# Kernel tuning notes

Hardware: AMD Instinct MI355X
Metric: run time of the kernel (lower is better)

Reference implementation:

```python
import jax, jax.numpy as jnp
import numpy as np
import math

D = 768      # d_model
H = 12       # heads
DH = D // H  # per-head dim
HID = 3072   # ffn hidden
L = 6        # layers each for encoder/decoder
S = 1024     # encoder seq len
T = 1024     # decoder seq len
MAXLEN = 1024


def pos_encoding(d, length):
    # pe[pos, 2i] = sin(pos / scale**i), pe[pos, 2i+1] = cos(pos / scale**i), scale = 1000**(2/d)
    scale = 1000.0 ** (2.0 / d)
    inv = scale ** (-np.arange(d // 2, dtype=np.float64))
    ang = np.arange(length, dtype=np.float64)[:, None] * inv[None, :]
    pe = np.zeros((length, d), dtype=np.float32)
    pe[:, 0::2] = np.sin(ang)
    pe[:, 1::2] = np.cos(ang)
    return jnp.asarray(pe)


def setup_inputs() -> dict:
    key = jax.random.key(0)
    ks = iter(jax.random.split(key, 64))
    def nrm(shape, s=0.02):
        return jax.random.normal(next(ks), shape, dtype=jnp.float32) * s
    inp = {
        'xl': nrm((S, D), 1.0),
        'dl': nrm((T, D), 1.0),
        'pos_enc': pos_encoding(D, MAXLEN),
        # encoder params (stacked over L layers, heads stacked over H)
        'enc_wq': nrm((L, H, DH, D)), 'enc_wk': nrm((L, H, DH, D)), 'enc_wv': nrm((L, H, DH, D)),
        'enc_wo': nrm((L, D, D)), 'enc_bo': jnp.zeros((L, D), jnp.float32),
        'enc_ln_a': jnp.ones((L, 2, D), jnp.float32), 'enc_ln_b': jnp.zeros((L, 2, D), jnp.float32),
        'enc_w1': nrm((L, HID, D)), 'enc_b1': jnp.zeros((L, HID), jnp.float32),
        'enc_w2': nrm((L, D, HID)), 'enc_b2': jnp.zeros((L, D), jnp.float32),
        # decoder self-attention
        'dec_wq': nrm((L, H, DH, D)), 'dec_wk': nrm((L, H, DH, D)), 'dec_wv': nrm((L, H, DH, D)),
        'dec_wo': nrm((L, D, D)), 'dec_bo': jnp.zeros((L, D), jnp.float32),
        # decoder cross-attention
        'dec_cwq': nrm((L, H, DH, D)), 'dec_cwk': nrm((L, H, DH, D)), 'dec_cwv': nrm((L, H, DH, D)),
        'dec_cwo': nrm((L, D, D)), 'dec_cbo': jnp.zeros((L, D), jnp.float32),
        'dec_ln_a': jnp.ones((L, 3, D), jnp.float32), 'dec_ln_b': jnp.zeros((L, 3, D), jnp.float32),
        'dec_w1': nrm((L, HID, D)), 'dec_b1': jnp.zeros((L, HID), jnp.float32),
        'dec_w2': nrm((L, D, HID)), 'dec_b2': jnp.zeros((L, D), jnp.float32),
    }
    return inp


def _ln_res(x, fx, a, b, eps=1e-6):
    # x = x + fx; a*(x-mean)/(std+eps)+b with UNBIASED std (torch default) and std (not var) in denom
    x = x + fx
    m = x.mean(-1, keepdims=True)
    s = jnp.std(x, axis=-1, keepdims=True, ddof=1)
    return a * (x - m) / (s + eps) + b


def _mha(qx, kx, vx, wq, wk, wv, wo, bo, mask=None):
    q = jnp.einsum('sd,hed->hse', qx, wq)  # [H,S,dh]
    k = jnp.einsum('td,hed->hte', kx, wk)
    v = jnp.einsum('td,hed->hte', vx, wv)
    scores = jnp.einsum('hse,hte->hst', q, k) / math.sqrt(q.shape[-1])
    if mask is not None:
        scores = scores + mask
    p = jax.nn.softmax(scores, axis=-1)  # softmax over keys (torch dim=1 on 2D scores)
    o = jnp.einsum('hst,hte->hse', p, v)
    o = jnp.transpose(o, (1, 0, 2)).reshape(qx.shape[0], -1)  # concat heads
    return o @ wo.T + bo


def _ffn(x, w1, b1, w2, b2):
    return jax.nn.relu(x @ w1.T + b1) @ w2.T + b2


def reference(xl, dl, pos_enc, enc_wq, enc_wk, enc_wv, enc_wo, enc_bo, enc_ln_a, enc_ln_b,
              enc_w1, enc_b1, enc_w2, enc_b2,
              dec_wq, dec_wk, dec_wv, dec_wo, dec_bo,
              dec_cwq, dec_cwk, dec_cwv, dec_cwo, dec_cbo,
              dec_ln_a, dec_ln_b, dec_w1, dec_b1, dec_w2, dec_b2):
    m = xl + pos_enc[: xl.shape[0]]
    for l in range(L):
        fx = _mha(m, m, m, enc_wq[l], enc_wk[l], enc_wv[l], enc_wo[l], enc_bo[l])
        m = _ln_res(m, fx, enc_ln_a[l, 0], enc_ln_b[l, 0])
        fx = _ffn(m, enc_w1[l], enc_b1[l], enc_w2[l], enc_b2[l])
        m = _ln_res(m, fx, enc_ln_a[l, 1], enc_ln_b[l, 1])
    n = dl.shape[0]
    # additive causal mask: -10000 where j > i
    cmask = -10000.0 * (jnp.arange(n)[None, :] > jnp.arange(n)[:, None]).astype(jnp.float32)
    out = dl + pos_enc[:n]
    for l in range(L):
        fx = _mha(out, out, out, dec_wq[l], dec_wk[l], dec_wv[l], dec_wo[l], dec_bo[l], cmask)
        out = _ln_res(out, fx, dec_ln_a[l, 0], dec_ln_b[l, 0])
        fx = _mha(out, m, m, dec_cwq[l], dec_cwk[l], dec_cwv[l], dec_cwo[l], dec_cbo[l])
        out = _ln_res(out, fx, dec_ln_a[l, 1], dec_ln_b[l, 1])
        fx = _ffn(out, dec_w1[l], dec_b1[l], dec_w2[l], dec_b2[l])
        out = _ln_res(out, fx, dec_ln_a[l, 2], dec_ln_b[l, 2])
    return jax.nn.softmax(out, axis=1)
```

## Files before the change

### kernel.cpp

```cpp
#include <hip/hip_runtime.h>
#include <math.h>

#define DMODEL 768
#define NHEAD 12
#define DHEAD 64
#define HIDDEN 3072
#define NLAYER 6
#define SEQ 1024
#define AC_ELEMS (SEQ * DMODEL)

typedef unsigned short u16;
typedef __attribute__((ext_vector_type(8))) short short8;
typedef __attribute__((ext_vector_type(4))) float f32x4;

__device__ __forceinline__ u16 f2bf(float f) {
    union { float f; unsigned u; } v; v.f = f;
    unsigned u = v.u;
    return (u16)((u + 0x7fffu + ((u >> 16) & 1u)) >> 16);
}
__device__ __forceinline__ float bf2f(u16 b) {
    union { unsigned u; float f; } v; v.u = ((unsigned)b) << 16; return v.f;
}

__device__ __forceinline__ void async16(const void* g, void* l) {
    __builtin_amdgcn_global_load_lds(
        (const __attribute__((address_space(1))) unsigned int*)g,
        (__attribute__((address_space(3))) unsigned int*)l, 16, 0, 0);
}

template<int N> __device__ __forceinline__ void waitv() {
    asm volatile("s_waitcnt vmcnt(%0)" :: "n"(N) : "memory");
    __builtin_amdgcn_sched_barrier(0);
}
__device__ __forceinline__ void drain_all() {
    asm volatile("s_waitcnt vmcnt(0) lgkmcnt(0)" ::: "memory");
    __builtin_amdgcn_sched_barrier(0);
}
__device__ __forceinline__ void bar() {
    __builtin_amdgcn_sched_barrier(0);
    __builtin_amdgcn_s_barrier();
    __builtin_amdgcn_sched_barrier(0);
}

__device__ __forceinline__ float block_sum(float v, float* red) {
    int tid = threadIdx.x;
    red[tid] = v;
    __syncthreads();
#pragma unroll
    for (int s = 128; s > 0; s >>= 1) {
        if (tid < s) red[tid] += red[tid + s];
        __syncthreads();
    }
    float r = red[0];
    __syncthreads();
    return r;
}
__device__ __forceinline__ float block_max(float v, float* red) {
    int tid = threadIdx.x;
    red[tid] = v;
    __syncthreads();
#pragma unroll
    for (int s = 128; s > 0; s >>= 1) {
        if (tid < s) red[tid] = fmaxf(red[tid], red[tid + s]);
        __syncthreads();
    }
    float r = red[0];
    __syncthreads();
    return r;
}

__global__ __launch_bounds__(256) void add_pe(const float* __restrict__ a,
                                              const float* __restrict__ b,
                                              float* __restrict__ o,
                                              u16* __restrict__ ob, int n) {
    int i = blockIdx.x * 256 + threadIdx.x;
    if (i < n) { float v = a[i] + b[i]; o[i] = v; ob[i] = f2bf(v); }
}

__global__ __launch_bounds__(256) void cvt_bf16(const float* __restrict__ src,
                                                u16* __restrict__ dst,
                                                long long per, long long sls, long long dls) {
    long long i = ((long long)blockIdx.x * 256 + threadIdx.x) * 4;
    if (i >= per) return;
    const float* s = src + (long long)blockIdx.y * sls + i;
    u16* d = dst + (long long)blockIdx.y * dls + i;
    float4 v = *(const float4*)s;
    ushort4 o;
    o.x = f2bf(v.x); o.y = f2bf(v.y); o.z = f2bf(v.z); o.w = f2bf(v.w);
    *(ushort4*)d = o;
}

template<int TM, int TN, int WR, int WC>
__global__ __launch_bounds__(WR * WC * 64) void gemm_mfma(
    const u16* __restrict__ A, int lda,
    const void* __restrict__ Bp, int ldb, int b_f32,
    const float* __restrict__ bias,
    void* __restrict__ Cp, int ldc, int c_bf16,
    float* __restrict__ C2,
    u16* __restrict__ vt_out, int vt_col0,
    int Ksub, int relu)
{
    constexpr int T  = WR * WC * 64;
    constexpr bool MW = (WR * WC) > 1;
    constexpr int FM = TM / (WR * 16), FN = TN / (WC * 16);
    constexpr int NA = TM * 8 / T, NB = TN * 8 / T;
    constexpr int LPS = NA + NB;
    __shared__ __align__(16) u16 As[3][TM * 64];
    __shared__ __align__(16) u16 Bs[3][TN * 64];

    const int zs = blockIdx.z;
    const u16*   B16 = (const u16*)Bp   + (long long)zs * Ksub;
    const float* B32 = (const float*)Bp + (long long)zs * Ksub;
    A += (long long)zs * Ksub;
    u16*   C16 = (u16*)Cp;
    float* C32 = (float*)Cp;

    const int t = threadIdx.x, lane = t & 63, w = t >> 6;
    const int wy = w / WC, wx = w % WC;
    const int n0 = blockIdx.y * TM, m0 = blockIdx.x * TN;

    auto stage = [&](int b, int k0) {
#pragma unroll
        for (int i = 0; i < NA; ++i) {
            int L = i * T + t;
            int row = L >> 3, cp = L & 7, c = cp ^ (row & 7);
            async16(A + (long long)(n0 + row) * lda + k0 + (c << 3),
                    &As[b][(i * T + w * 64) * 8]);
        }
        if (!b_f32) {
#pragma unroll
            for (int i = 0; i < NB; ++i) {
                int L = i * T + t;
                int row = L >> 3, cp = L & 7, c = cp ^ (row & 7);
                async16(B16 + (long long)(m0 + row) * ldb + k0 + (c << 3),
                        &Bs[b][(i * T + w * 64) * 8]);
            }
        } else {
#pragma unroll
            for (int i = 0; i < NB; ++i) {
                int L = i * T + t;
                int row = L >> 3, cp = L & 7, c = cp ^ (row & 7);
                const float* s = B32 + (long long)(m0 + row) * ldb + k0 + (c << 3);
                float4 x = *(const float4*)s;
                float4 y = *(const float4*)(s + 4);
                uint4 pk;
                pk.x = (unsigned)f2bf(x.x) | ((unsigned)f2bf(x.y) << 16);
                pk.y = (unsigned)f2bf(x.z) | ((unsigned)f2bf(x.w) << 16);
                pk.z = (unsigned)f2bf(y.x) | ((unsigned)f2bf(y.y) << 16);
                pk.w = (unsigned)f2bf(y.z) | ((unsigned)f2bf(y.w) << 16);
                *(uint4*)&Bs[b][row * 64 + cp * 8] = pk;
            }
        }
    };

    const int nk = Ksub / 64;
    stage(0, 0);
    if (nk > 1) stage(1, 64);

    f32x4 acc[FM][FN] = {};

    for (int tt = 0; tt < nk; ++tt) {
        if (tt + 2 < nk) stage((tt + 2) % 3, (tt + 2) * 64);
        if (b_f32)             drain_all();
        else if (tt + 2 < nk)  waitv<2 * LPS>();
        else if (tt + 1 < nk)  waitv<LPS>();
        else                   waitv<0>();
        if (MW) bar();

        const u16* Ac = As[tt % 3];
        const u16* Bc = Bs[tt % 3];
#pragma unroll
        for (int kk = 0; kk < 2; ++kk) {
            short8 af[FM], bfv[FN];
            const int cb = kk * 4 + (lane >> 4);
#pragma unroll
            for (int m = 0; m < FM; ++m) {
                int R = wy * (TM / WR) + m * 16 + (lane & 15);
                af[m] = *(const short8*)&Ac[R * 64 + ((cb ^ (R & 7)) << 3)];
            }
#pragma unroll
            for (int n = 0; n < FN; ++n) {
                int R = wx * (TN / WC) + n * 16 + (lane & 15);
                bfv[n] = *(const short8*)&Bc[R * 64 + ((cb ^ (R & 7)) << 3)];
            }
#pragma unroll
            for (int m = 0; m < FM; ++m)
#pragma unroll
                for (int n = 0; n < FN; ++n)
                    acc[m][n] = __builtin_amdgcn_mfma_f32_16x16x32_bf16(af[m], bfv[n], acc[m][n], 0, 0, 0);
        }
        if (MW) bar();
    }

    const int cj = lane & 15, ci0 = (lane >> 4) << 2;
    const bool z0 = (zs == 0);
#pragma unroll
    for (int m = 0; m < FM; ++m) {
#pragma unroll
        for (int n = 0; n < FN; ++n) {
            int col = m0 + wx * (TN / WC) + n * 16 + cj;
            bool to_vt = z0 && vt_out && (col >= vt_col0);
            float bv = (z0 && bias) ? bias[col] : 0.0f;
#pragma unroll
            for (int r = 0; r < 4; ++r) {
                int row = n0 + wy * (TM / WR) + m * 16 + ci0 + r;
                float v = acc[m][n][r] + bv;
                if (relu) v = fmaxf(v, 0.0f);
                if (!z0)          C2[(long long)row * ldc + col] = v;
                else if (to_vt)   vt_out[(long long)(col - vt_col0) * SEQ + row] = f2bf(v);
                else if (c_bf16)  C16[(long long)row * ldc + col] = f2bf(v);
                else              C32[(long long)row * ldc + col] = v;
            }
        }
    }
}

template<int CAUSAL>
__global__ __launch_bounds__(256) void attn_split(
    const u16* __restrict__ Qg,
    const u16* __restrict__ Kg,
    const u16* __restrict__ VT,
    float* __restrict__ Op,
    float* __restrict__ Ml)
{
    const int h  = blockIdx.y;
    const int qt = blockIdx.x;
    const int s  = blockIdx.z;
    const int q0 = qt * 64;
    const int t = threadIdx.x, lane = t & 63, w = t >> 6;

    const int last = CAUSAL ? qt : (SEQ / 64 - 1);

    if (CAUSAL && s > last) {
        for (int e = t; e < 64 * 64; e += 256) {
            int r = e >> 6, c = e & 63;
            Op[(long long)s * AC_ELEMS + (long long)(q0 + r) * DMODEL + h * 64 + c] = 0.0f;
        }
        if (t < 64) {
            long long mi = (((long long)s * NHEAD + h) * SEQ + q0 + t) * 2;
            Ml[mi] = -3.0e38f; Ml[mi + 1] = 0.0f;
        }
        return;
    }

    __shared__ __align__(16) u16 Ks[2][64 * 64];
    __shared__ __align__(16) u16 Vs[2][64 * 64];
    __shared__ __align__(16) u16 Ps[4][16 * 64];

    short8 qf[2];
    {
        int qrow = q0 + w * 16 + (lane & 15);
        const u16* qp = Qg + (long long)qrow * (3 * DMODEL) + h * DHEAD + ((lane >> 4) << 3);
        qf[0] = *(const short8*)qp;
        qf[1] = *(const short8*)(qp + 32);
    }

    auto stage = [&](int b, int kt) {
#pragma unroll
        for (int i = 0; i < 2; ++i) {
            int LL = i * 256 + t;
            int row = LL >> 3, cp = LL & 7, c = cp ^ (row & 7);
            async16(Kg + (long long)(kt * 64 + row) * (3 * DMODEL) + h * DHEAD + (c << 3),
                    &Ks[b][(i * 256 + w * 64) * 8]);
            async16(VT + (long long)(h * DHEAD + row) * SEQ + kt * 64 + (c << 3),
                    &Vs[b][(i * 256 + w * 64) * 8]);
        }
    };

    f32x4 o_acc[4] = {};
    float m_r[4], l_r[4];
#pragma unroll
    for (int r = 0; r < 4; ++r) { m_r[r] = -3.0e38f; l_r[r] = 0.f; }

    stage(0, s);

    int buf = 0;
    for (int kt = s; kt <= last; kt += 2) {
        if (kt + 2 <= last) { stage(buf ^ 1, kt + 2); waitv<4>(); }
        else                { waitv<0>(); }
        bar();

        f32x4 sv[4] = {};
#pragma unroll
        for (int kk = 0; kk < 2; ++kk) {
            const int cb = kk * 4 + (lane >> 4);
#pragma unroll
            for (int n = 0; n < 4; ++n) {
                int R = n * 16 + (lane & 15);
                short8 kf = *(const short8*)&Ks[buf][R * 64 + ((cb ^ (R & 7)) << 3)];
                sv[n] = __builtin_amdgcn_mfma_f32_16x16x32_bf16(qf[kk], kf, sv[n], 0, 0, 0);
            }
        }

#pragma unroll
        for (int n = 0; n < 4; ++n) {
            int keyl = n * 16 + (lane & 15);
#pragma unroll
            for (int r = 0; r < 4; ++r) {
                float v = sv[n][r] * 0.125f;
                if (CAUSAL && kt == qt) {
                    int ql = w * 16 + ((lane >> 4) << 2) + r;
                    if (keyl > ql) v -= 10000.0f;
                }
                sv[n][r] = v;
            }
        }

#pragma unroll
        for (int r = 0; r < 4; ++r) {
            float vm = fmaxf(fmaxf(sv[0][r], sv[1][r]), fmaxf(sv[2][r], sv[3][r]));
            vm = fmaxf(vm, __shfl_xor(vm, 1));
            vm = fmaxf(vm, __shfl_xor(vm, 2));
            vm = fmaxf(vm, __shfl_xor(vm, 4));
            vm = fmaxf(vm, __shfl_xor(vm, 8));
            float mn = fmaxf(m_r[r], vm);
            float sf = __expf(m_r[r] - mn);
            m_r[r] = mn;
            float rowsum = 0.f;
#pragma unroll
            for (int n = 0; n < 4; ++n) {
                float p = __expf(sv[n][r] - mn);
                sv[n][r] = p;
                rowsum += p;
            }
            rowsum += __shfl_xor(rowsum, 1);
            rowsum += __shfl_xor(rowsum, 2);
            rowsum += __shfl_xor(rowsum, 4);
            rowsum += __shfl_xor(rowsum, 8);
            l_r[r] = l_r[r] * sf + rowsum;
#pragma unroll
            for (int d = 0; d < 4; ++d) o_acc[d][r] *= sf;
        }

#pragma unroll
        for (int n = 0; n < 4; ++n) {
            int jh = lane & 7;
            int chunk = n * 2 + ((lane & 15) >> 3);
#pragma unroll
            for (int r = 0; r < 4; ++r) {
                int q = ((lane >> 4) << 2) + r;
                Ps[w][q * 64 + ((chunk ^ (q & 7)) << 3) + jh] = f2bf(sv[n][r]);
            }
        }

#pragma unroll
        for (int kk = 0; kk < 2; ++kk) {
            int q = lane & 15;
            int chunk = (lane >> 4) + kk * 4;
            short8 pf = *(const short8*)&Ps[w][q * 64 + ((chunk ^ (q & 7)) << 3)];
            const int cb = kk * 4 + (lane >> 4);
#pragma unroll
            for (int d = 0; d < 4; ++d) {
                int R = d * 16 + (lane & 15);
                short8 vf = *(const short8*)&Vs[buf][R * 64 + ((cb ^ (R & 7)) << 3)];
                o_acc[d] = __builtin_amdgcn_mfma_f32_16x16x32_bf16(pf, vf, o_acc[d], 0, 0, 0);
            }
        }
        bar();
        buf ^= 1;
    }

#pragma unroll
    for (int r = 0; r < 4; ++r) {
        int row = q0 + w * 16 + ((lane >> 4) << 2) + r;
#pragma unroll
        for (int d = 0; d < 4; ++d) {
            int col = h * DHEAD + d * 16 + (lane & 15);
            Op[(long long)s * AC_ELEMS + (long long)row * DMODEL + col] = o_acc[d][r];
        }
        if ((lane & 15) == 0) {
            long long mi = (((long long)s * NHEAD + h) * SEQ + row) * 2;
            Ml[mi] = m_r[r]; Ml[mi + 1] = l_r[r];
        }
    }
}

__global__ __launch_bounds__(192) void attn_combine(const float* __restrict__ Op,
                                                    const float* __restrict__ Ml,
                                                    u16* __restrict__ O) {
    const int row = blockIdx.x;
    const int c0 = threadIdx.x * 4;
    const int h = c0 >> 6;
    long long m0i = (((long long)0 * NHEAD + h) * SEQ + row) * 2;
    long long m1i = (((long long)1 * NHEAD + h) * SEQ + row) * 2;
    float m0 = Ml[m0i], l0 = Ml[m0i + 1];
    float m1 = Ml[m1i], l1 = Ml[m1i + 1];
    float M = fmaxf(m0, m1);
    float w0 = __expf(m0 - M), w1 = __expf(m1 - M);
    float inv = 1.0f / (w0 * l0 + w1 * l1);
    float4 a = *(const float4*)&Op[(long long)row * DMODEL + c0];
    float4 b = *(const float4*)&Op[(long long)AC_ELEMS + (long long)row * DMODEL + c0];
    ushort4 o;
    o.x = f2bf((w0 * a.x + w1 * b.x) * inv);
    o.y = f2bf((w0 * a.y + w1 * b.y) * inv);
    o.z = f2bf((w0 * a.z + w1 * b.z) * inv);
    o.w = f2bf((w0 * a.w + w1 * b.w) * inv);
    *(ushort4*)&O[(long long)row * DMODEL + c0] = o;
}

__global__ __launch_bounds__(256) void softmax_f32(const float* __restrict__ in,
                                                   float* __restrict__ out, int width) {
    const float* row = in + (long long)blockIdx.x * width;
    float* orow = out + (long long)blockIdx.x * width;
    int tid = threadIdx.x;
    __shared__ float red[256];
    int nf4 = width >> 2;
    float4 v = {-1e30f, -1e30f, -1e30f, -1e30f};
    if (tid < nf4) v = ((const float4*)row)[tid];
    float mx = fmaxf(fmaxf(v.x, v.y), fmaxf(v.z, v.w));
    mx = block_max(mx, red);
    float4 e = {0.f, 0.f, 0.f, 0.f};
    float s = 0.f;
    if (tid < nf4) {
        e.x = __expf(v.x - mx); e.y = __expf(v.y - mx);
        e.z = __expf(v.z - mx); e.w = __expf(v.w - mx);
        s = e.x + e.y + e.z + e.w;
    }
    s = block_sum(s, red);
    float inv = 1.0f / s;
    if (tid < nf4) {
        e.x *= inv; e.y *= inv; e.z *= inv; e.w *= inv;
        ((float4*)orow)[tid] = e;
    }
}

__global__ __launch_bounds__(256) void ln_res_kernel(float* __restrict__ x,
                                                     const float* __restrict__ fx,
                                                     const float* __restrict__ fx2,
                                                     const float* __restrict__ ga,
                                                     const float* __restrict__ gb,
                                                     u16* __restrict__ xb) {
    long long row = blockIdx.x;
    float* xr = x + row * DMODEL;
    const float* fr = fx + row * DMODEL;
    u16* xbr = xb + row * DMODEL;
    int tid = threadIdx.x;
    __shared__ float red[256];

    float4 tv = {0.f, 0.f, 0.f, 0.f};
    if (tid < 192) {
        float4 a = ((const float4*)xr)[tid];
        float4 f = ((const float4*)fr)[tid];
        tv.x = a.x + f.x; tv.y = a.y + f.y; tv.z = a.z + f.z; tv.w = a.w + f.w;
        if (fx2) {
            float4 g = ((const float4*)(fx2 + row * DMODEL))[tid];
            tv.x += g.x; tv.y += g.y; tv.z += g.z; tv.w += g.w;
        }
    }
    float sum = tv.x + tv.y + tv.z + tv.w;
    sum = block_sum(sum, red);
    float mean = sum * (1.0f / (float)DMODEL);

    float4 d = {0.f, 0.f, 0.f, 0.f};
    float ss = 0.f;
    if (tid < 192) {
        d.x = tv.x - mean; d.y = tv.y - mean; d.z = tv.z - mean; d.w = tv.w - mean;
        ss = d.x * d.x + d.y * d.y + d.z * d.z + d.w * d.w;
    }
    ss = block_sum(ss, red);
    float stdv = sqrtf(ss / (float)(DMODEL - 1));
    float inv = 1.0f / (stdv + 1e-6f);

    if (tid < 192) {
        float4 A = ((const float4*)ga)[tid];
        float4 B = ((const float4*)gb)[tid];
        float4 o;
        o.x = A.x * d.x * inv + B.x;
        o.y = A.y * d.y * inv + B.y;
        o.z = A.z * d.z * inv + B.z;
        o.w = A.w * d.w * inv + B.w;
        ((float4*)xr)[tid] = o;
        ushort4 ob;
        ob.x = f2bf(o.x); ob.y = f2bf(o.y); ob.z = f2bf(o.z); ob.w = f2bf(o.w);
        ((ushort4*)xbr)[tid] = ob;
    }
}

struct GArg {
    const u16* A; int lda;
    const void* B; int ldb; int b_f32;
    const float* bias;
    void* C; int ldc; int c_bf16;
    u16* vt; int vt_col0;
    int N, M, K; int relu;
};
template<int TM, int TN, int WR, int WC>
static inline void glaunch(hipStream_t st, const GArg& a, int splitk = 1, float* C2 = nullptr) {
    dim3 grid(a.M / TN, a.N / TM, splitk);
    hipLaunchKernelGGL((gemm_mfma<TM, TN, WR, WC>), grid, dim3(WR * WC * 64), 0, st,
                       a.A, a.lda, a.B, a.ldb, a.b_f32, a.bias, a.C, a.ldc, a.c_bf16,
                       C2, a.vt, a.vt_col0, a.K / splitk, a.relu);
}

extern "C" void kernel_launch(void* const* d_in, const int* in_sizes, int n_in,
                              void* d_out, int out_size, void* d_ws, size_t ws_size,
                              hipStream_t stream) {
    const float* xl      = (const float*)d_in[0];
    const float* dl      = (const float*)d_in[1];
    const float* pe      = (const float*)d_in[2];
    const float* enc_wq  = (const float*)d_in[3];
    const float* enc_wk  = (const float*)d_in[4];
    const float* enc_wv  = (const float*)d_in[5];
    const float* enc_wo  = (const float*)d_in[6];
    const float* enc_bo  = (const float*)d_in[7];
    const float* enc_lna = (const float*)d_in[8];
    const float* enc_lnb = (const float*)d_in[9];
    const float* enc_w1  = (const float*)d_in[10];
    const float* enc_b1  = (const float*)d_in[11];
    const float* enc_w2  = (const float*)d_in[12];
    const float* enc_b2  = (const float*)d_in[13];
    const float* dec_wq  = (const float*)d_in[14];
    const float* dec_wk  = (const float*)d_in[15];
    const float* dec_wv  = (const float*)d_in[16];
    const float* dec_wo  = (const float*)d_in[17];
    const float* dec_bo  = (const float*)d_in[18];
    const float* dec_cwq = (const float*)d_in[19];
    const float* dec_cwk = (const float*)d_in[20];
    const float* dec_cwv = (const float*)d_in[21];
    const float* dec_cwo = (const float*)d_in[22];
    const float* dec_cbo = (const float*)d_in[23];
    const float* dec_lna = (const float*)d_in[24];
    const float* dec_lnb = (const float*)d_in[25];
    const float* dec_w1  = (const float*)d_in[26];
    const float* dec_b1  = (const float*)d_in[27];
    const float* dec_w2  = (const float*)d_in[28];
    const float* dec_b2  = (const float*)d_in[29];

    const long long AC   = AC_ELEMS;
    const long long DD   = (long long)DMODEL * DMODEL;
    const long long WH   = (long long)HIDDEN * DMODEL;
    const long long QKVC = (long long)SEQ * 3 * DMODEL;
    const long long SH   = (long long)SEQ * HIDDEN;

    float* mbuf  = (float*)d_ws;
    float* xbuf  = mbuf + AC;
    float* fbuf  = xbuf + AC;
    float* fbuf2 = fbuf + AC;
    float* Opart = fbuf2 + AC;
    float* Ml    = Opart + 2 * AC;
    u16* u = (u16*)(Ml + 2LL * NHEAD * SEQ * 2);
    u16* mb16 = u;  u += AC;
    u16* xb16 = u;  u += AC;
    u16* qkvb = u;  u += QKVC;
    u16* vt   = u;  u += AC;
    u16* ob   = u;  u += AC;
    u16* hb   = u;  u += SH;

    u16* W = u;
    long long woff = 0;
    const long long W_ENC_QKV = woff; woff += 18 * DD;
    const long long W_ENC_WO  = woff; woff += 6 * DD;
    const long long W_ENC_W1  = woff; woff += 6 * WH;
    const long long W_ENC_W2  = woff; woff += 6 * WH;
    const long long W_DEC_QKV = woff; woff += 18 * DD;
    const long long W_DEC_CQKV= woff; woff += 18 * DD;
    const long long W_DEC_WO  = woff; woff += 6 * DD;
    const long long W_DEC_CWO = woff; woff += 6 * DD;
    const long long W_DEC_W1  = woff; woff += 6 * WH;
    const long long W_DEC_W2  = woff; woff += 6 * WH;
    const long long need = (long long)((char*)(W + woff) - (char*)d_ws);
    const bool conv = ((long long)ws_size >= need);

    if (conv) {
        auto cvt = [&](const float* src, long long dst_off, long long per, long long sls, long long dls, int L) {
            dim3 grid((unsigned)((per / 4 + 255) / 256), L);
            hipLaunchKernelGGL(cvt_bf16, grid, dim3(256), 0, stream, src, W + dst_off, per, sls, dls);
        };
        cvt(enc_wq, W_ENC_QKV + 0 * DD, DD, DD, 3 * DD, NLAYER);
        cvt(enc_wk, W_ENC_QKV + 1 * DD, DD, DD, 3 * DD, NLAYER);
        cvt(enc_wv, W_ENC_QKV + 2 * DD, DD, DD, 3 * DD, NLAYER);
        cvt(enc_wo, W_ENC_WO, 6 * DD, 0, 0, 1);
        cvt(enc_w1, W_ENC_W1, 6 * WH, 0, 0, 1);
        cvt(enc_w2, W_ENC_W2, 6 * WH, 0, 0, 1);
        cvt(dec_wq, W_DEC_QKV + 0 * DD, DD, DD, 3 * DD, NLAYER);
        cvt(dec_wk, W_DEC_QKV + 1 * DD, DD, DD, 3 * DD, NLAYER);
        cvt(dec_wv, W_DEC_QKV + 2 * DD, DD, DD, 3 * DD, NLAYER);
        cvt(dec_cwq, W_DEC_CQKV + 0 * DD, DD, DD, 3 * DD, NLAYER);
        cvt(dec_cwk, W_DEC_CQKV + 1 * DD, DD, DD, 3 * DD, NLAYER);
        cvt(dec_cwv, W_DEC_CQKV + 2 * DD, DD, DD, 3 * DD, NLAYER);
        cvt(dec_wo, W_DEC_WO, 6 * DD, 0, 0, 1);
        cvt(dec_cwo, W_DEC_CWO, 6 * DD, 0, 0, 1);
        cvt(dec_w1, W_DEC_W1, 6 * WH, 0, 0, 1);
        cvt(dec_w2, W_DEC_W2, 6 * WH, 0, 0, 1);
    }

    hipLaunchKernelGGL(add_pe, dim3((int)(AC / 256)), dim3(256), 0, stream, xl, pe, mbuf, mb16, (int)AC);

    auto attn = [&](int causal) {
        dim3 grid(SEQ / 64, NHEAD, 2);
        if (causal)
            hipLaunchKernelGGL((attn_split<1>), grid, dim3(256), 0, stream,
                               qkvb, qkvb + DMODEL, vt, Opart, Ml);
        else
            hipLaunchKernelGGL((attn_split<0>), grid, dim3(256), 0, stream,
                               qkvb, qkvb + DMODEL, vt, Opart, Ml);
        hipLaunchKernelGGL(attn_combine, dim3(SEQ), dim3(192), 0, stream, Opart, Ml, ob);
    };

    for (int l = 0; l < NLAYER; ++l) {
        if (conv) {
            GArg qkv = { mb16, DMODEL, W + W_ENC_QKV + l * 3 * DD, DMODEL, 0, nullptr,
                         qkvb, 3 * DMODEL, 1, vt, 2 * DMODEL, SEQ, 3 * DMODEL, DMODEL, 0 };
            glaunch<64, 64, 2, 2>(stream, qkv);
        } else {
            const float* wps[3] = { enc_wq + l * DD, enc_wk + l * DD, enc_wv + l * DD };
            for (int j = 0; j < 3; ++j) {
                GArg a = { mb16, DMODEL, wps[j], DMODEL, 1, nullptr,
                           qkvb + j * DMODEL, 3 * DMODEL, 1,
                           (j == 2) ? vt : nullptr, 0, SEQ, DMODEL, DMODEL, 0 };
                glaunch<32, 32, 1, 1>(stream, a);
            }
        }
        attn(0);
        GArg wo = { ob, DMODEL,
                    conv ? (const void*)(W + W_ENC_WO + l * DD) : (const void*)(enc_wo + l * DD),
                    DMODEL, conv ? 0 : 1, enc_bo + (long long)l * DMODEL,
                    fbuf, DMODEL, 0, nullptr, 0, SEQ, DMODEL, DMODEL, 0 };
        glaunch<32, 32, 1, 1>(stream, wo);
        hipLaunchKernelGGL(ln_res_kernel, dim3(SEQ), dim3(256), 0, stream,
                           mbuf, fbuf, (const float*)nullptr,
                           enc_lna + (long long)(l * 2 + 0) * DMODEL,
                           enc_lnb + (long long)(l * 2 + 0) * DMODEL, mb16);
        GArg f1 = { mb16, DMODEL,
                    conv ? (const void*)(W + W_ENC_W1 + l * WH) : (const void*)(enc_w1 + l * WH),
                    DMODEL, conv ? 0 : 1, enc_b1 + (long long)l * HIDDEN,
                    hb, HIDDEN, 1, nullptr, 0, SEQ, HIDDEN, DMODEL, 1 };
        glaunch<64, 64, 2, 2>(stream, f1);
        GArg f2 = { hb, HIDDEN,
                    conv ? (const void*)(W + W_ENC_W2 + l * WH) : (const void*)(enc_w2 + l * WH),
                    HIDDEN, conv ? 0 : 1, enc_b2 + (long long)l * DMODEL,
                    fbuf, DMODEL, 0, nullptr, 0, SEQ, DMODEL, HIDDEN, 0 };
        glaunch<64, 64, 2, 2>(stream, f2, 2, fbuf2);
        hipLaunchKernelGGL(ln_res_kernel, dim3(SEQ), dim3(256), 0, stream,
                           mbuf, fbuf, fbuf2,
                           enc_lna + (long long)(l * 2 + 1) * DMODEL,
                           enc_lnb + (long long)(l * 2 + 1) * DMODEL, mb16);
    }

    hipLaunchKernelGGL(add_pe, dim3((int)(AC / 256)), dim3(256), 0, stream, dl, pe, xbuf, xb16, (int)AC);

    for (int l = 0; l < NLAYER; ++l) {
        if (conv) {
            GArg qkv = { xb16, DMODEL, W + W_DEC_QKV + l * 3 * DD, DMODEL, 0, nullptr,
                         qkvb, 3 * DMODEL, 1, vt, 2 * DMODEL, SEQ, 3 * DMODEL, DMODEL, 0 };
            glaunch<64, 64, 2, 2>(stream, qkv);
        } else {
            const float* wps[3] = { dec_wq + l * DD, dec_wk + l * DD, dec_wv + l * DD };
            for (int j = 0; j < 3; ++j) {
                GArg a = { xb16, DMODEL, wps[j], DMODEL, 1, nullptr,
                           qkvb + j * DMODEL, 3 * DMODEL, 1,
                           (j == 2) ? vt : nullptr, 0, SEQ, DMODEL, DMODEL, 0 };
                glaunch<32, 32, 1, 1>(stream, a);
            }
        }
        attn(1);
        GArg wo = { ob, DMODEL,
                    conv ? (const void*)(W + W_DEC_WO + l * DD) : (const void*)(dec_wo + l * DD),
                    DMODEL, conv ? 0 : 1, dec_bo + (long long)l * DMODEL,
                    fbuf, DMODEL, 0, nullptr, 0, SEQ, DMODEL, DMODEL, 0 };
        glaunch<32, 32, 1, 1>(stream, wo);
        hipLaunchKernelGGL(ln_res_kernel, dim3(SEQ), dim3(256), 0, stream,
                           xbuf, fbuf, (const float*)nullptr,
                           dec_lna + (long long)(l * 3 + 0) * DMODEL,
                           dec_lnb + (long long)(l * 3 + 0) * DMODEL, xb16);

        if (conv) {
            GArg q = { xb16, DMODEL, W + W_DEC_CQKV + l * 3 * DD, DMODEL, 0, nullptr,
                       qkvb, 3 * DMODEL, 1, nullptr, 0, SEQ, DMODEL, DMODEL, 0 };
            glaunch<32, 32, 1, 1>(stream, q);
            GArg kv = { mb16, DMODEL, W + W_DEC_CQKV + l * 3 * DD + DD, DMODEL, 0, nullptr,
                        qkvb + DMODEL, 3 * DMODEL, 1, vt, DMODEL, SEQ, 2 * DMODEL, DMODEL, 0 };
            glaunch<32, 32, 1, 1>(stream, kv);
        } else {
            GArg q = { xb16, DMODEL, dec_cwq + l * DD, DMODEL, 1, nullptr,
                       qkvb, 3 * DMODEL, 1, nullptr, 0, SEQ, DMODEL, DMODEL, 0 };
            glaunch<32, 32, 1, 1>(stream, q);
            GArg ck = { mb16, DMODEL, dec_cwk + l * DD, DMODEL, 1, nullptr,
                        qkvb + DMODEL, 3 * DMODEL, 1, nullptr, 0, SEQ, DMODEL, DMODEL, 0 };
            glaunch<32, 32, 1, 1>(stream, ck);
            GArg cv = { mb16, DMODEL, dec_cwv + l * DD, DMODEL, 1, nullptr,
                        qkvb + 2 * DMODEL, 3 * DMODEL, 1, vt, 0, SEQ, DMODEL, DMODEL, 0 };
            glaunch<32, 32, 1, 1>(stream, cv);
        }
        attn(0);
        GArg cwo = { ob, DMODEL,
                     conv ? (const void*)(W + W_DEC_CWO + l * DD) : (const void*)(dec_cwo + l * DD),
                     DMODEL, conv ? 0 : 1, dec_cbo + (long long)l * DMODEL,
                     fbuf, DMODEL, 0, nullptr, 0, SEQ, DMODEL, DMODEL, 0 };
        glaunch<32, 32, 1, 1>(stream, cwo);
        hipLaunchKernelGGL(ln_res_kernel, dim3(SEQ), dim3(256), 0, stream,
                           xbuf, fbuf, (const float*)nullptr,
                           dec_lna + (long long)(l * 3 + 1) * DMODEL,
                           dec_lnb + (long long)(l * 3 + 1) * DMODEL, xb16);

        GArg f1 = { xb16, DMODEL,
                    conv ? (const void*)(W + W_DEC_W1 + l * WH) : (const void*)(dec_w1 + l * WH),
                    DMODEL, conv ? 0 : 1, dec_b1 + (long long)l * HIDDEN,
                    hb, HIDDEN, 1, nullptr, 0, SEQ, HIDDEN, DMODEL, 1 };
        glaunch<64, 64, 2, 2>(stream, f1);
        GArg f2 = { hb, HIDDEN,
                    conv ? (const void*)(W + W_DEC_W2 + l * WH) : (const void*)(dec_w2 + l * WH),
                    HIDDEN, conv ? 0 : 1, dec_b2 + (long long)l * DMODEL,
                    fbuf, DMODEL, 0, nullptr, 0, SEQ, DMODEL, HIDDEN, 0 };
        glaunch<64, 64, 2, 2>(stream, f2, 2, fbuf2);
        hipLaunchKernelGGL(ln_res_kernel, dim3(SEQ), dim3(256), 0, stream,
                           xbuf, fbuf, fbuf2,
                           dec_lna + (long long)(l * 3 + 2) * DMODEL,
                           dec_lnb + (long long)(l * 3 + 2) * DMODEL, xb16);
    }

    hipLaunchKernelGGL(softmax_f32, dim3(SEQ), dim3(256), 0, stream, xbuf, (float*)d_out, DMODEL);
}
```

Measured before the change: 1.750 ms.

## Fuse split-attention combine into output projection and batch cross-attention K/V GEMMs

The separate attn_combine kernel is removed. The Wo/CWo GEMM now loads both fp32 attention partials and their max/sum stats, merges and normalises them, and converts to bf16 while staging its A tile. The cross-attention K/V projections for all six decoder layers are computed up front as one wide GEMM over the encoder output, writing V transposed per layer. This saves many launches and round trips through intermediate buffers. In exchange, the fused A staging is synchronous (it drains all loads each step), reads twice the fp32 data, and adds larger K/V buffers.

```diff
diff --git a/kernel.cpp b/kernel.cpp
--- a/kernel.cpp
+++ b/kernel.cpp
@@ -97,7 +97,8 @@
     const float* __restrict__ bias,
     void* __restrict__ Cp, int ldc, int c_bf16,
     float* __restrict__ C2,
-    u16* __restrict__ vt_out, int vt_col0,
+    u16* __restrict__ vt_out, int vt_col0, int vt_mode,
+    const float* __restrict__ Aop, const float* __restrict__ Aml,
     int Ksub, int relu)
 {
     constexpr int T  = WR * WC * 64;
@@ -118,14 +119,51 @@
     const int t = threadIdx.x, lane = t & 63, w = t >> 6;
     const int wy = w / WC, wx = w % WC;
     const int n0 = blockIdx.y * TM, m0 = blockIdx.x * TN;
+    const bool slow = (b_f32 != 0) || (Aop != nullptr);
 
     auto stage = [&](int b, int k0) {
-#pragma unroll
-        for (int i = 0; i < NA; ++i) {
-            int L = i * T + t;
-            int row = L >> 3, cp = L & 7, c = cp ^ (row & 7);
-            async16(A + (long long)(n0 + row) * lda + k0 + (c << 3),
-                    &As[b][(i * T + w * 64) * 8]);
+        if (!Aop) {
+#pragma unroll
+            for (int i = 0; i < NA; ++i) {
+                int L = i * T + t;
+                int row = L >> 3, cp = L & 7, c = cp ^ (row & 7);
+                async16(A + (long long)(n0 + row) * lda + k0 + (c << 3),
+                        &As[b][(i * T + w * 64) * 8]);
+            }
+        } else {
+#pragma unroll
+            for (int i = 0; i < NA; ++i) {
+                int L = i * T + t;
+                int row = L >> 3, cp = L & 7, c = cp ^ (row & 7);
+                int grow = n0 + row;
+                int gk = k0 + (c << 3);
+                int h = gk >> 6;
+                const float* q0 = Aml + (((long long)h * SEQ + grow) << 1);
+                const float* q1 = Aml + (((long long)(NHEAD + h) * SEQ + grow) << 1);
+                float m0v = q0[0], l0v = q0[1];
+                float m1v = q1[0], l1v = q1[1];
+                float M = fmaxf(m0v, m1v);
+                float w0 = __expf(m0v - M), w1 = __expf(m1v - M);
+                float inv = 1.0f / (w0 * l0v + w1 * l1v);
+                const float* p0 = Aop + (long long)grow * DMODEL + gk;
+                const float* p1 = p0 + AC_ELEMS;
+                float4 x0 = *(const float4*)p0, y0 = *(const float4*)(p0 + 4);
+                float4 x1 = *(const float4*)p1, y1 = *(const float4*)(p1 + 4);
+                float a0 = (w0 * x0.x + w1 * x1.x) * inv;
+                float a1 = (w0 * x0.y + w1 * x1.y) * inv;
+                float a2 = (w0 * x0.z + w1 * x1.z) * inv;
+                float a3 = (w0 * x0.w + w1 * x1.w) * inv;
+                float a4 = (w0 * y0.x + w1 * y1.x) * inv;
+                float a5 = (w0 * y0.y + w1 * y1.y) * inv;
+                float a6 = (w0 * y0.z + w1 * y1.z) * inv;
+                float a7 = (w0 * y0.w + w1 * y1.w) * inv;
+                uint4 pk;
+                pk.x = (unsigned)f2bf(a0) | ((unsigned)f2bf(a1) << 16);
+                pk.y = (unsigned)f2bf(a2) | ((unsigned)f2bf(a3) << 16);
+                pk.z = (unsigned)f2bf(a4) | ((unsigned)f2bf(a5) << 16);
+                pk.w = (unsigned)f2bf(a6) | ((unsigned)f2bf(a7) << 16);
+                *(uint4*)&As[b][row * 64 + cp * 8] = pk;
+            }
         }
         if (!b_f32) {
 #pragma unroll
@@ -161,7 +199,7 @@
 
     for (int tt = 0; tt < nk; ++tt) {
         if (tt + 2 < nk) stage((tt + 2) % 3, (tt + 2) * 64);
-        if (b_f32)             drain_all();
+        if (slow)              drain_all();
         else if (tt + 2 < nk)  waitv<2 * LPS>();
         else if (tt + 1 < nk)  waitv<LPS>();
         else                   waitv<0>();
@@ -194,22 +232,28 @@
 
     const int cj = lane & 15, ci0 = (lane >> 4) << 2;
     const bool z0 = (zs == 0);
+    float* C2z = C2 + (long long)(zs - 1) * AC_ELEMS;
 #pragma unroll
     for (int m = 0; m < FM; ++m) {
 #pragma unroll
         for (int n = 0; n < FN; ++n) {
             int col = m0 + wx * (TN / WC) + n * 16 + cj;
-            bool to_vt = z0 && vt_out && (col >= vt_col0);
             float bv = (z0 && bias) ? bias[col] : 0.0f;
+            long long vtidx = -1;
+            if (z0 && vt_mode == 1 && col >= vt_col0) vtidx = (long long)(col - vt_col0) * SEQ;
+            else if (z0 && vt_mode == 2) {
+                int blk = col / 1536, rem = col % 1536;
+                if (rem >= 768) vtidx = ((long long)blk * 768 + rem - 768) * SEQ;
+            }
 #pragma unroll
             for (int r = 0; r < 4; ++r) {
                 int row = n0 + wy * (TM / WR) + m * 16 + ci0 + r;
                 float v = acc[m][n][r] + bv;
                 if (relu) v = fmaxf(v, 0.0f);
-                if (!z0)          C2[(long long)row * ldc + col] = v;
-                else if (to_vt)   vt_out[(long long)(col - vt_col0) * SEQ + row] = f2bf(v);
-                else if (c_bf16)  C16[(long long)row * ldc + col] = f2bf(v);
-                else              C32[(long long)row * ldc + col] = v;
+                if (!z0)            C2z[(long long)row * ldc + col] = v;
+                else if (vtidx >= 0) vt_out[vtidx + row] = f2bf(v);
+                else if (c_bf16)    C16[(long long)row * ldc + col] = f2bf(v);
+                else                C32[(long long)row * ldc + col] = v;
             }
         }
     }
@@ -217,8 +261,8 @@
 
 template<int CAUSAL>
 __global__ __launch_bounds__(256) void attn_split(
-    const u16* __restrict__ Qg,
-    const u16* __restrict__ Kg,
+    const u16* __restrict__ Qg, int ldq,
+    const u16* __restrict__ Kg, int ldk,
     const u16* __restrict__ VT,
     float* __restrict__ Op,
     float* __restrict__ Ml)
@@ -250,7 +294,7 @@
     short8 qf[2];
     {
         int qrow = q0 + w * 16 + (lane & 15);
-        const u16* qp = Qg + (long long)qrow * (3 * DMODEL) + h * DHEAD + ((lane >> 4) << 3);
+        const u16* qp = Qg + (long long)qrow * ldq + h * DHEAD + ((lane >> 4) << 3);
         qf[0] = *(const short8*)qp;
         qf[1] = *(const short8*)(qp + 32);
     }
@@ -260,7 +304,7 @@
         for (int i = 0; i < 2; ++i) {
             int LL = i * 256 + t;
             int row = LL >> 3, cp = LL & 7, c = cp ^ (row & 7);
-            async16(Kg + (long long)(kt * 64 + row) * (3 * DMODEL) + h * DHEAD + (c << 3),
+            async16(Kg + (long long)(kt * 64 + row) * ldk + h * DHEAD + (c << 3),
                     &Ks[b][(i * 256 + w * 64) * 8]);
             async16(VT + (long long)(h * DHEAD + row) * SEQ + kt * 64 + (c << 3),
                     &Vs[b][(i * 256 + w * 64) * 8]);
@@ -373,29 +417,6 @@
             Ml[mi] = m_r[r]; Ml[mi + 1] = l_r[r];
         }
     }
-}
-
-__global__ __launch_bounds__(192) void attn_combine(const float* __restrict__ Op,
-                                                    const float* __restrict__ Ml,
-                                                    u16* __restrict__ O) {
-    const int row = blockIdx.x;
-    const int c0 = threadIdx.x * 4;
-    const int h = c0 >> 6;
-    long long m0i = (((long long)0 * NHEAD + h) * SEQ + row) * 2;
-    long long m1i = (((long long)1 * NHEAD + h) * SEQ + row) * 2;
-    float m0 = Ml[m0i], l0 = Ml[m0i + 1];
-    float m1 = Ml[m1i], l1 = Ml[m1i + 1];
-    float M = fmaxf(m0, m1);
-    float w0 = __expf(m0 - M), w1 = __expf(m1 - M);
-    float inv = 1.0f / (w0 * l0 + w1 * l1);
-    float4 a = *(const float4*)&Op[(long long)row * DMODEL + c0];
-    float4 b = *(const float4*)&Op[(long long)AC_ELEMS + (long long)row * DMODEL + c0];
-    ushort4 o;
-    o.x = f2bf((w0 * a.x + w1 * b.x) * inv);
-    o.y = f2bf((w0 * a.y + w1 * b.y) * inv);
-    o.z = f2bf((w0 * a.z + w1 * b.z) * inv);
-    o.w = f2bf((w0 * a.w + w1 * b.w) * inv);
-    *(ushort4*)&O[(long long)row * DMODEL + c0] = o;
 }
 
 __global__ __launch_bounds__(256) void softmax_f32(const float* __restrict__ in,
@@ -427,6 +448,7 @@
 __global__ __launch_bounds__(256) void ln_res_kernel(float* __restrict__ x,
                                                      const float* __restrict__ fx,
                                                      const float* __restrict__ fx2,
+                                                     int n2,
                                                      const float* __restrict__ ga,
                                                      const float* __restrict__ gb,
                                                      u16* __restrict__ xb) {
@@ -442,8 +464,8 @@
         float4 a = ((const float4*)xr)[tid];
         float4 f = ((const float4*)fr)[tid];
         tv.x = a.x + f.x; tv.y = a.y + f.y; tv.z = a.z + f.z; tv.w = a.w + f.w;
-        if (fx2) {
-            float4 g = ((const float4*)(fx2 + row * DMODEL))[tid];
+        for (int j = 0; j < n2; ++j) {
+            float4 g = ((const float4*)(fx2 + (long long)j * AC_ELEMS + row * DMODEL))[tid];
             tv.x += g.x; tv.y += g.y; tv.z += g.z; tv.w += g.w;
         }
     }
@@ -481,7 +503,8 @@
     const void* B; int ldb; int b_f32;
     const float* bias;
     void* C; int ldc; int c_bf16;
-    u16* vt; int vt_col0;
+    u16* vt; int vt_col0; int vt_mode;
+    const float* Aop; const float* Aml;
     int N, M, K; int relu;
 };
 template<int TM, int TN, int WR, int WC>
@@ -489,7 +512,7 @@
     dim3 grid(a.M / TN, a.N / TM, splitk);
     hipLaunchKernelGGL((gemm_mfma<TM, TN, WR, WC>), grid, dim3(WR * WC * 64), 0, st,
                        a.A, a.lda, a.B, a.ldb, a.b_f32, a.bias, a.C, a.ldc, a.c_bf16,
-                       C2, a.vt, a.vt_col0, a.K / splitk, a.relu);
+                       C2, a.vt, a.vt_col0, a.vt_mode, a.Aop, a.Aml, a.K / splitk, a.relu);
 }
 
 extern "C" void kernel_launch(void* const* d_in, const int* in_sizes, int n_in,
@@ -543,8 +566,9 @@
     u16* xb16 = u;  u += AC;
     u16* qkvb = u;  u += QKVC;
     u16* vt   = u;  u += AC;
-    u16* ob   = u;  u += AC;
     u16* hb   = u;  u += SH;
+    u16* ckb  = u;  u += 12LL * AC;
+    u16* cvb  = u;  u += 6LL * AC;
 
     u16* W = u;
     long long woff = 0;
@@ -553,7 +577,8 @@
     const long long W_ENC_W1  = woff; woff += 6 * WH;
     const long long W_ENC_W2  = woff; woff += 6 * WH;
     const long long W_DEC_QKV = woff; woff += 18 * DD;
-    const long long W_DEC_CQKV= woff; woff += 18 * DD;
+    const long long W_DEC_CQ  = woff; woff += 6 * DD;
+    const long long W_DEC_CKV = woff; woff += 12 * DD;
     const long long W_DEC_WO  = woff; woff += 6 * DD;
     const long long W_DEC_CWO = woff; woff += 6 * DD;
     const long long W_DEC_W1  = woff; woff += 6 * WH;
@@ -575,9 +600,9 @@
         cvt(dec_wq, W_DEC_QKV + 0 * DD, DD, DD, 3 * DD, NLAYER);
         cvt(dec_wk, W_DEC_QKV + 1 * DD, DD, DD, 3 * DD, NLAYER);
         cvt(dec_wv, W_DEC_QKV + 2 * DD, DD, DD, 3 * DD, NLAYER);
-        cvt(dec_cwq, W_DEC_CQKV + 0 * DD, DD, DD, 3 * DD, NLAYER);
-        cvt(dec_cwk, W_DEC_CQKV + 1 * DD, DD, DD, 3 * DD, NLAYER);
-        cvt(dec_cwv, W_DEC_CQKV + 2 * DD, DD, DD, 3 * DD, NLAYER);
+        cvt(dec_cwq, W_DEC_CQ, 6 * DD, 0, 0, 1);
+        cvt(dec_cwk, W_DEC_CKV + 0 * DD, DD, DD, 2 * DD, NLAYER);
+        cvt(dec_cwv, W_DEC_CKV + 1 * DD, DD, DD, 2 * DD, NLAYER);
         cvt(dec_wo, W_DEC_WO, 6 * DD, 0, 0, 1);
         cvt(dec_cwo, W_DEC_CWO, 6 * DD, 0, 0, 1);
         cvt(dec_w1, W_DEC_W1, 6 * WH, 0, 0, 1);
@@ -586,55 +611,64 @@
 
     hipLaunchKernelGGL(add_pe, dim3((int)(AC / 256)), dim3(256), 0, stream, xl, pe, mbuf, mb16, (int)AC);
 
-    auto attn = [&](int causal) {
+    auto attn = [&](int causal, const u16* Qg, int ldq, const u16* Kg, int ldk, const u16* VT) {
         dim3 grid(SEQ / 64, NHEAD, 2);
         if (causal)
-            hipLaunchKernelGGL((attn_split<1>), grid, dim3(256), 0, stream,
-                               qkvb, qkvb + DMODEL, vt, Opart, Ml);
+            hipLaunchKernelGGL((attn_split<1>), grid, dim3(256), 0, stream, Qg, ldq, Kg, ldk, VT, Opart, Ml);
         else
-            hipLaunchKernelGGL((attn_split<0>), grid, dim3(256), 0, stream,
-                               qkvb, qkvb + DMODEL, vt, Opart, Ml);
-        hipLaunchKernelGGL(attn_combine, dim3(SEQ), dim3(192), 0, stream, Opart, Ml, ob);
+            hipLaunchKernelGGL((attn_split<0>), grid, dim3(256), 0, stream, Qg, ldq, Kg, ldk, VT, Opart, Ml);
     };
 
     for (int l = 0; l < NLAYER; ++l) {
         if (conv) {
             GArg qkv = { mb16, DMODEL, W + W_ENC_QKV + l * 3 * DD, DMODEL, 0, nullptr,
-                         qkvb, 3 * DMODEL, 1, vt, 2 * DMODEL, SEQ, 3 * DMODEL, DMODEL, 0 };
+                         qkvb, 3 * DMODEL, 1, vt, 2 * DMODEL, 1, nullptr, nullptr,
+                         SEQ, 3 * DMODEL, DMODEL, 0 };
             glaunch<64, 64, 2, 2>(stream, qkv);
         } else {
             const float* wps[3] = { enc_wq + l * DD, enc_wk + l * DD, enc_wv + l * DD };
             for (int j = 0; j < 3; ++j) {
                 GArg a = { mb16, DMODEL, wps[j], DMODEL, 1, nullptr,
                            qkvb + j * DMODEL, 3 * DMODEL, 1,
-                           (j == 2) ? vt : nullptr, 0, SEQ, DMODEL, DMODEL, 0 };
+                           (j == 2) ? vt : nullptr, 0, (j == 2) ? 1 : 0, nullptr, nullptr,
+                           SEQ, DMODEL, DMODEL, 0 };
                 glaunch<32, 32, 1, 1>(stream, a);
             }
         }
-        attn(0);
-        GArg wo = { ob, DMODEL,
+        attn(0, qkvb, 3 * DMODEL, qkvb + DMODEL, 3 * DMODEL, vt);
+        GArg wo = { nullptr, 0,
                     conv ? (const void*)(W + W_ENC_WO + l * DD) : (const void*)(enc_wo + l * DD),
                     DMODEL, conv ? 0 : 1, enc_bo + (long long)l * DMODEL,
-                    fbuf, DMODEL, 0, nullptr, 0, SEQ, DMODEL, DMODEL, 0 };
+                    fbuf, DMODEL, 0, nullptr, 0, 0, Opart, Ml,
+                    SEQ, DMODEL, DMODEL, 0 };
         glaunch<32, 32, 1, 1>(stream, wo);
         hipLaunchKernelGGL(ln_res_kernel, dim3(SEQ), dim3(256), 0, stream,
-                           mbuf, fbuf, (const float*)nullptr,
+                           mbuf, fbuf, (const float*)nullptr, 0,
                            enc_lna + (long long)(l * 2 + 0) * DMODEL,
                            enc_lnb + (long long)(l * 2 + 0) * DMODEL, mb16);
         GArg f1 = { mb16, DMODEL,
                     conv ? (const void*)(W + W_ENC_W1 + l * WH) : (const void*)(enc_w1 + l * WH),
                     DMODEL, conv ? 0 : 1, enc_b1 + (long long)l * HIDDEN,
-                    hb, HIDDEN, 1, nullptr, 0, SEQ, HIDDEN, DMODEL, 1 };
+                    hb, HIDDEN, 1, nullptr, 0, 0, nullptr, nullptr,
+                    SEQ, HIDDEN, DMODEL, 1 };
         glaunch<64, 64, 2, 2>(stream, f1);
         GArg f2 = { hb, HIDDEN,
                     conv ? (const void*)(W + W_ENC_W2 + l * WH) : (const void*)(enc_w2 + l * WH),
                     HIDDEN, conv ? 0 : 1, enc_b2 + (long long)l * DMODEL,
-                    fbuf, DMODEL, 0, nullptr, 0, SEQ, DMODEL, HIDDEN, 0 };
+                    fbuf, DMODEL, 0, nullptr, 0, 0, nullptr, nullptr,
+                    SEQ, DMODEL, HIDDEN, 0 };
         glaunch<64, 64, 2, 2>(stream, f2, 2, fbuf2);
         hipLaunchKernelGGL(ln_res_kernel, dim3(SEQ), dim3(256), 0, stream,
-                           mbuf, fbuf, fbuf2,
+                           mbuf, fbuf, fbuf2, 1,
                            enc_lna + (long long)(l * 2 + 1) * DMODEL,
                            enc_lnb + (long long)(l * 2 + 1) * DMODEL, mb16);
+    }
+
+    if (conv) {
+        GArg ckv = { mb16, DMODEL, W + W_DEC_CKV, DMODEL, 0, nullptr,
+                     ckb, 12 * DMODEL, 1, cvb, 0, 2, nullptr, nullptr,
+                     SEQ, 12 * DMODEL, DMODEL, 0 };
+        glaunch<64, 64, 2, 2>(stream, ckv);
     }
 
     hipLaunchKernelGGL(add_pe, dim3((int)(AC / 256)), dim3(256), 0, stream, dl, pe, xbuf, xb16, (int)AC);
@@ -642,69 +676,77 @@
     for (int l = 0; l < NLAYER; ++l) {
         if (conv) {
             GArg qkv = { xb16, DMODEL, W + W_DEC_QKV + l * 3 * DD, DMODEL, 0, nullptr,
-                         qkvb, 3 * DMODEL, 1, vt, 2 * DMODEL, SEQ, 3 * DMODEL, DMODEL, 0 };
+                         qkvb, 3 * DMODEL, 1, vt, 2 * DMODEL, 1, nullptr, nullptr,
+                         SEQ, 3 * DMODEL, DMODEL, 0 };
             glaunch<64, 64, 2, 2>(stream, qkv);
         } else {
             const float* wps[3] = { dec_wq + l * DD, dec_wk + l * DD, dec_wv + l * DD };
             for (int j = 0; j < 3; ++j) {
                 GArg a = { xb16, DMODEL, wps[j], DMODEL, 1, nullptr,
                            qkvb + j * DMODEL, 3 * DMODEL, 1,
-                           (j == 2) ? vt : nullptr, 0, SEQ, DMODEL, DMODEL, 0 };
+                           (j == 2) ? vt : nullptr, 0, (j == 2) ? 1 : 0, nullptr, nullptr,
+                           SEQ, DMODEL, DMODEL, 0 };
                 glaunch<32, 32, 1, 1>(stream, a);
             }
         }
-        attn(1);
-        GArg wo = { ob, DMODEL,
+        attn(1, qkvb, 3 * DMODEL, qkvb + DMODEL, 3 * DMODEL, vt);
+        GArg wo = { nullptr, 0,
                     conv ? (const void*)(W + W_DEC_WO + l * DD) : (const void*)(dec_wo + l * DD),
                     DMODEL, conv ? 0 : 1, dec_bo + (long long)l * DMODEL,
-                    fbuf, DMODEL, 0, nullptr, 0, SEQ, DMODEL, DMODEL, 0 };
+                    fbuf, DMODEL, 0, nullptr, 0, 0, Opart, Ml,
+                    SEQ, DMODEL, DMODEL, 0 };
         glaunch<32, 32, 1, 1>(stream, wo);
         hipLaunchKernelGGL(ln_res_kernel, dim3(SEQ), dim3(256), 0, stream,
-                           xbuf, fbuf, (const float*)nullptr,
+                           xbuf, fbuf, (const float*)nullptr, 0,
                            dec_lna + (long long)(l * 3 + 0) * DMODEL,
                            dec_lnb + (long long)(l * 3 + 0) * DMODEL, xb16);
 
         if (conv) {
-            GArg q = { xb16, DMODEL, W + W_DEC_CQKV + l * 3 * DD, DMODEL, 0, nullptr,
-                       qkvb, 3 * DMODEL, 1, nullptr, 0, SEQ, DMODEL, DMODEL, 0 };
+            GArg q = { xb16, DMODEL, W + W_DEC_CQ + l * DD, DMODEL, 0, nullptr,
+                       qkvb, 3 * DMODEL, 1, nullptr, 0, 0, nullptr, nullptr,
+                       SEQ, DMODEL, DMODEL, 0 };
             glaunch<32, 32, 1, 1>(stream, q);
-            GArg kv = { mb16, DMODEL, W + W_DEC_CQKV + l * 3 * DD + DD, DMODEL, 0, nullptr,
-                        qkvb + DMODEL, 3 * DMODEL, 1, vt, DMODEL, SEQ, 2 * DMODEL, DMODEL, 0 };
-            glaunch<32, 32, 1, 1>(stream, kv);
+            attn(0, qkvb, 3 * DMODEL, ckb + l * 2 * DMODEL, 12 * DMODEL, cvb + (long long)l * AC);
         } else {
             GArg q = { xb16, DMODEL, dec_cwq + l * DD, DMODEL, 1, nullptr,
-                       qkvb, 3 * DMODEL, 1, nullptr, 0, SEQ, DMODEL, DMODEL, 0 };
+                       qkvb, 3 * DMODEL, 1, nullptr, 0, 0, nullptr, nullptr,
+                       SEQ, DMODEL, DMODEL, 0 };
             glaunch<32, 32, 1, 1>(stream, q);
             GArg ck = { mb16, DMODEL, dec_cwk + l * DD, DMODEL, 1, nullptr,
-                        qkvb + DMODEL, 3 * DMODEL, 1, nullptr, 0, SEQ, DMODEL, DMODEL, 0 };
+                        qkvb + DMODEL, 3 * DMODEL, 1, nullptr, 0, 0, nullptr, nullptr,
+                        SEQ, DMODEL, DMODEL, 0 };
             glaunch<32, 32, 1, 1>(stream, ck);
             GArg cv = { mb16, DMODEL, dec_cwv + l * DD, DMODEL, 1, nullptr,
-                        qkvb + 2 * DMODEL, 3 * DMODEL, 1, vt, 0, SEQ, DMODEL, DMODEL, 0 };
+                        qkvb + 2 * DMODEL, 3 * DMODEL, 1, vt, 0, 1, nullptr, nullptr,
+                        SEQ, DMODEL, DMODEL, 0 };
             glaunch<32, 32, 1, 1>(stream, cv);
-        }
-        attn(0);
-        GArg cwo = { ob, DMODEL,
+            attn(0, qkvb, 3 * DMODEL, qkvb + DMODEL, 3 * DMODEL, vt);
+        }
+        GArg cwo = { nullptr, 0,
                      conv ? (const void*)(W + W_DEC_CWO + l * DD) : (const void*)(dec_cwo + l * DD),
                      DMODEL, conv ? 0 : 1, dec_cbo + (long long)l * DMODEL,
-                     fbuf, DMODEL, 0, nullptr, 0, SEQ, DMODEL, DMODEL, 0 };
+                     fbuf, DMODEL, 0, nullptr, 0, 0, Opart, Ml,
+                     SEQ, DMODEL, DMODEL, 0 };
         glaunch<32, 32, 1, 1>(stream, cwo);
         hipLaunchKernelGGL(ln_res_kernel, dim3(SEQ), dim3(256), 0, stream,
-                           xbuf, fbuf, (const float*)nullptr,
+                           xbuf, fbuf, (const float*)nullptr, 0,
                            dec_lna + (long long)(l * 3 + 1) * DMODEL,
                            dec_lnb + (long long)(l * 3 + 1) * DMODEL, xb16);
 
         GArg f1 = { xb16, DMODEL,
                     conv ? (const void*)(W + W_DEC_W1 + l * WH) : (const void*)(dec_w1 + l * WH),
                     DMODEL, conv ? 0 : 1, dec_b1 + (long long)l * HIDDEN,
-                    hb, HIDDEN, 1, nullptr, 0, SEQ, HIDDEN, DMODEL, 1 };
+                    hb, HIDDEN, 1, nullptr, 0, 0, nullptr, nullptr,
+                    SEQ, HIDDEN, DMODEL, 1 };
         glaunch<64, 64, 2, 2>(stream, f1);
         GArg f2 = { hb, HIDDEN,
                     conv ? (const void*)(W + W_DEC_W2 + l * WH) : (const void*)(dec_w2 + l * WH),
                     HIDDEN, conv ? 0 : 1, dec_b2 + (long long)l * DMODEL,
-                    fbuf, DMODEL, 0, nullptr, 0, SEQ, DMODEL, HIDDEN, 0 };
+                    fbuf, DMODEL, 0, nullptr, 0, 0, nullptr, nullptr,
+                    SEQ, DMODEL, HIDDEN, 0 };
         glaunch<64, 64, 2, 2>(stream, f2, 2, fbuf2);
         hipLaunchKernelGGL(ln_res_kernel, dim3(SEQ), dim3(256), 0, stream,
-                           xbuf, fbuf, fbuf2,
+                           xbuf, fbuf, fbuf2, 1,
                            dec_lna + (long long)(l * 3 + 2) * DMODEL,
                            dec_lnb + (long long)(l * 3 + 2) * DMODEL, xb16);
     }
```

Result: slower. 2.017 ms (+15.2%).
